# Optimization experiments

Hardware: AMD Instinct MI355X
Metric: run time of the kernel (lower is better)

Reference implementation:

```python
import jax, jax.numpy as jnp
import numpy as np

B, L, D, H, T = 1024, 50, 4, 512, 30


def _lstm_cell(x, h, c, W_ih, W_hh, b_ih, b_hh):
    # PyTorch LSTM gate order: i, f, g, o
    g = x @ W_ih.T + b_ih + h @ W_hh.T + b_hh
    i, f, gg, o = jnp.split(g, 4, axis=-1)
    c = jax.nn.sigmoid(f) * c + jax.nn.sigmoid(i) * jnp.tanh(gg)
    h = jax.nn.sigmoid(o) * jnp.tanh(c)
    return h, c


def setup_inputs() -> dict:
    key = jax.random.key(0)
    ks = jax.random.split(key, 16)
    s = 0.05
    return {
        "input_tensor": jax.random.normal(ks[0], (B, L, D), jnp.float32),
        "target_len": T,
        "enc_W_ih": jax.random.normal(ks[1], (4 * H, D), jnp.float32) * s,
        "enc_W_hh": jax.random.normal(ks[2], (4 * H, H), jnp.float32) * s,
        "enc_b_ih": jax.random.normal(ks[3], (4 * H,), jnp.float32) * s,
        "enc_b_hh": jax.random.normal(ks[4], (4 * H,), jnp.float32) * s,
        "attn_W": jax.random.normal(ks[5], (L, H + D), jnp.float32) * s,
        "attn_b": jax.random.normal(ks[6], (L,), jnp.float32) * s,
        "comb_W": jax.random.normal(ks[7], (H, H + D), jnp.float32) * s,
        "comb_b": jax.random.normal(ks[8], (H,), jnp.float32) * s,
        "dec_W_ih": jax.random.normal(ks[9], (4 * H, H), jnp.float32) * s,
        "dec_W_hh": jax.random.normal(ks[10], (4 * H, H), jnp.float32) * s,
        "dec_b_ih": jax.random.normal(ks[11], (4 * H,), jnp.float32) * s,
        "dec_b_hh": jax.random.normal(ks[12], (4 * H,), jnp.float32) * s,
        "out_W": jax.random.normal(ks[13], (D, H), jnp.float32) * s,
        "out_b": jax.random.normal(ks[14], (D,), jnp.float32) * s,
    }


def reference(input_tensor, target_len, enc_W_ih, enc_W_hh, enc_b_ih, enc_b_hh,
              attn_W, attn_b, comb_W, comb_b,
              dec_W_ih, dec_W_hh, dec_b_ih, dec_b_hh, out_W, out_b):
    b = input_tensor.shape[0]

    # ---- encoder LSTM over input_len steps ----
    def enc_step(carry, x_t):
        h, c = carry
        h, c = _lstm_cell(x_t, h, c, enc_W_ih, enc_W_hh, enc_b_ih, enc_b_hh)
        return (h, c), h

    h0 = jnp.zeros((b, H), input_tensor.dtype)
    (h_enc, c_enc), enc_hs = jax.lax.scan(enc_step, (h0, h0),
                                          jnp.swapaxes(input_tensor, 0, 1))
    encoder_outputs = jnp.swapaxes(enc_hs, 0, 1)  # [B, L, H]

    # ---- recursive attention decoder over target_len steps ----
    def dec_step(carry, _):
        h, c, x = carry
        # faithful to torch: h.reshape(h.shape[1], -1).transpose(1, 0)
        h_r = jnp.transpose(h.reshape(H, -1))  # [B, H] (memory reinterpret)
        attn_logits = jnp.concatenate([x, h_r], axis=1) @ attn_W.T + attn_b
        attn_weights = jax.nn.softmax(attn_logits, axis=1)        # [B, L]
        attn_applied = jnp.einsum('bl,blh->bh', attn_weights, encoder_outputs)
        comb = jnp.concatenate([x, attn_applied], axis=1) @ comb_W.T + comb_b
        comb = jax.nn.relu(comb)                                  # [B, H]
        h, c = _lstm_cell(comb, h, c, dec_W_ih, dec_W_hh, dec_b_ih, dec_b_hh)
        pred = h @ out_W.T + out_b                                # [B, D]
        return (h, c, pred), pred

    dec_in0 = input_tensor[:, -1, :]
    _, preds = jax.lax.scan(dec_step, (h_enc, c_enc, dec_in0), None,
                            length=target_len)
    return jnp.swapaxes(preds, 0, 1)  # [B, target_len, D]
```

## Files before the change

kernel.cpp:

```cpp
#include <hip/hip_runtime.h>
#include <hip/hip_bf16.h>

#define Bsz   1024
#define Lseq  50
#define Din   4
#define Hd    512
#define Tlen  30

typedef __hip_bfloat16 bf16;
typedef short s16x8 __attribute__((ext_vector_type(8)));
typedef short s16x4 __attribute__((ext_vector_type(4)));
typedef float f32x4 __attribute__((ext_vector_type(4)));

__device__ __forceinline__ float bf2f(bf16 x){ return __bfloat162float(x); }
__device__ __forceinline__ bf16  f2bf(float x){ return __float2bfloat16(x); }
__device__ __forceinline__ float bfbits2f(short u){
    union { unsigned int ui; float f; } v;
    v.ui = ((unsigned int)(unsigned short)u) << 16;
    return v.f;
}
__device__ __forceinline__ short f2bfbits(float x){
    bf16 h = f2bf(x); short s; __builtin_memcpy(&s, &h, 2); return s;
}
__device__ __forceinline__ float sigm(float x){ return 1.0f/(1.0f + __expf(-x)); }

#define OFF_ABUF0   (0u)
#define OFF_ABUF1   (2u<<20)
#define OFF_CBUF    (4u<<20)
#define OFF_HF32    (6u<<20)
#define OFF_ATTNAP  (8u<<20)
#define OFF_XDEC    (9u<<20)
#define OFF_FLAG    ((9u<<20) + (16u<<10))
#define OFF_COMBWR  ((9u<<20) + (32u<<10))
#define OFF_ATTNWR  ((9u<<20) + (600u<<10))
#define OFF_WCACHE  (10u<<20)
#define OFF_ENCOUT  (18u<<20)

#define WC_INPUT 0
#define WC_EWIH  204800
#define WC_EWHH  212992
#define WC_EBIH  1261568
#define WC_EBHH  1263616
#define WC_AW    1265664
#define WC_AB    1291464
#define WC_CW    1291520
#define WC_CB    1555712
#define WC_DWIH  1556224
#define WC_DWHH  2604800
#define WC_DBIH  3653376
#define WC_DBHH  3655424
#define WC_OW    3657472
#define WC_OB    3659520
#define WC_TOTAL 3659524

__device__ __constant__ int WOFF[15] = {
    WC_INPUT, WC_EWIH, WC_EWHH, WC_EBIH, WC_EBHH, WC_AW, WC_AB, WC_CW,
    WC_CB, WC_DWIH, WC_DWHH, WC_DBIH, WC_DBHH, WC_OW, WC_OB };
__device__ __constant__ int WNUM[15] = {
    204800, 8192, 1048576, 2048, 2048, 25800, 50, 264192,
    512, 1048576, 1048576, 2048, 2048, 2048, 4 };

struct Ptrs15 { const void* p[15]; };

__global__ void probe_kernel(const unsigned int* __restrict__ w, int* flag){
    __shared__ int cnt;
    if (threadIdx.x == 0) cnt = 0;
    __syncthreads();
    int c = 0;
    for (int i = threadIdx.x; i < 4096; i += 256){
        unsigned e = (w[i] >> 7) & 0xFFu;
        c += (e >= 0x80u) ? 1 : 0;
    }
    atomicAdd(&cnt, c);
    __syncthreads();
    if (threadIdx.x == 0) *flag = (cnt > 400) ? 1 : 0;
}

__global__ __launch_bounds__(256) void convert_kernel(
    Ptrs15 srcs, const int* __restrict__ flag, bf16* __restrict__ dst)
{
    const int f = *flag;
    for (int idx = blockIdx.x*256 + threadIdx.x; idx < WC_TOTAL;
         idx += gridDim.x*256){
        int a = 0;
#pragma unroll
        for (int j = 1; j < 15; ++j) if (idx >= WOFF[j]) a = j;
        const int local = idx - WOFF[a];
        if (local >= WNUM[a]) continue;
        bf16 v;
        if (f) v = f2bf(((const float*)srcs.p[a])[local]);
        else   v = ((const bf16*)srcs.p[a])[local];
        dst[idx] = v;
    }
}

__global__ __launch_bounds__(256) void setup_kernel(
    bf16* __restrict__ Abuf0, bf16* __restrict__ Abuf1,
    float* __restrict__ cbuf, bf16* __restrict__ combWr,
    bf16* __restrict__ attnWr,
    const bf16* __restrict__ cWc, const bf16* __restrict__ aWc)
{
    const unsigned idx = blockIdx.x*256u + threadIdx.x;
    if (idx < (unsigned)Bsz*Hd){
        const unsigned row = idx >> 9, col = idx & (Hd-1);
        const bf16 z = f2bf(0.0f);
        Abuf0[(size_t)row*1024 + Hd + col] = z;
        Abuf1[(size_t)row*1024 + Hd + col] = z;
        cbuf[idx] = 0.0f;
    }
    if (idx < (unsigned)Hd*Hd)
        combWr[idx] = cWc[(size_t)(idx >> 9)*(Hd+Din) + Din + (idx & (Hd-1))];
    if (idx < (unsigned)Lseq*Hd)
        attnWr[idx] = aWc[(size_t)(idx >> 9)*(Hd+Din) + Din + (idx & (Hd-1))];
}

template<bool TWO, bool HASX, bool WENC>
__global__ __launch_bounds__(512, 2) void gates_kernel(
    const bf16* __restrict__ A, int lda,
    const bf16* __restrict__ W1, const bf16* __restrict__ W2,
    const bf16* __restrict__ bih, const bf16* __restrict__ bhh,
    const bf16* __restrict__ Wx,
    const bf16* __restrict__ xsrc, int ldx,
    float* __restrict__ cbuf,
    bf16* __restrict__ hout,
    bf16* __restrict__ hout2, int ldh2,
    float* __restrict__ hf32)
{
    const int wg = blockIdx.x;
    const int mt = wg >> 4, nt = wg & 15;
    const int bm0 = mt << 6, hc0 = nt << 5;
    const int tid = threadIdx.x;
    const int wave = tid >> 6, lane = tid & 63;
    const int wm = wave >> 1, wn = wave & 1;
    const int quad = lane >> 4, l15 = lane & 15;

    const int arow = bm0 + wm*16 + l15;
    int ng[4];
#pragma unroll
    for (int an = 0; an < 4; ++an){
        const int n = wn*64 + an*16 + l15;
        ng[an] = (n & 3)*Hd + hc0 + (n >> 2);
    }

    float bias[4];
#pragma unroll
    for (int an = 0; an < 4; ++an)
        bias[an] = bf2f(bih[ng[an]]) + bf2f(bhh[ng[an]]);
    float xv[4][4], wxv[4][4];
    if (HASX){
#pragma unroll
        for (int r = 0; r < 4; ++r){
            const int m = bm0 + wm*16 + quad*4 + r;
            const s16x4 t = *reinterpret_cast<const s16x4*>(xsrc + (size_t)m*ldx);
#pragma unroll
            for (int d = 0; d < 4; ++d) xv[r][d] = bfbits2f(t[d]);
        }
#pragma unroll
        for (int an = 0; an < 4; ++an){
            const s16x4 t = *reinterpret_cast<const s16x4*>(Wx + (size_t)ng[an]*Din);
#pragma unroll
            for (int d = 0; d < 4; ++d) wxv[an][d] = bfbits2f(t[d]);
        }
    }

    f32x4 acc[4];
#pragma unroll
    for (int an = 0; an < 4; ++an) acc[an] = (f32x4)0.0f;

    const bf16* Ab = A + (size_t)arow*lda + quad*8;
    const bf16* wbase[2] = { W1, W2 };
#pragma unroll
    for (int h = 0; h < (TWO ? 2 : 1); ++h){
        const bf16* Wb = wbase[h];
        const bf16* Ah = Ab + h*Hd;
#pragma unroll
        for (int kk = 0; kk < 16; ++kk){
            const int k = kk*32 + quad*8;
            s16x8 bfr[4];
#pragma unroll
            for (int an = 0; an < 4; ++an)
                bfr[an] = *reinterpret_cast<const s16x8*>(Wb + (size_t)ng[an]*Hd + k);
            const s16x8 afr = *reinterpret_cast<const s16x8*>(Ah + kk*32);
#pragma unroll
            for (int an = 0; an < 4; ++an)
                acc[an] = __builtin_amdgcn_mfma_f32_16x16x32_bf16(afr, bfr[an], acc[an], 0, 0, 0);
        }
    }

    const int lbase = lane & ~3;
#pragma unroll
    for (int an = 0; an < 4; ++an){
        const int n = wn*64 + an*16 + l15;
        const int hcol = hc0 + (n >> 2);
#pragma unroll
        for (int r = 0; r < 4; ++r){
            const int m = bm0 + wm*16 + quad*4 + r;
            float gv = acc[an][r] + bias[an];
            if (HASX)
                gv += xv[r][0]*wxv[an][0] + xv[r][1]*wxv[an][1]
                    + xv[r][2]*wxv[an][2] + xv[r][3]*wxv[an][3];
            const float gi = __shfl(gv, lbase+0);
            const float gf = __shfl(gv, lbase+1);
            const float gg = __shfl(gv, lbase+2);
            const float go = __shfl(gv, lbase+3);
            if ((lane & 3) == 0){
                const size_t ci = (size_t)m*Hd + hcol;
                const float cn = sigm(gf)*cbuf[ci] + sigm(gi)*tanhf(gg);
                cbuf[ci] = cn;
                const float hv = sigm(go)*tanhf(cn);
                const bf16 hb = f2bf(hv);
                hout[(size_t)m*1024 + hcol] = hb;
                hf32[ci] = hv;
                if (WENC) hout2[(size_t)m*ldh2 + hcol] = hb;
            }
        }
    }
}

__global__ __launch_bounds__(256) void comb_kernel(
    const bf16* __restrict__ A,
    const bf16* __restrict__ Wr,
    const bf16* __restrict__ combW,
    const bf16* __restrict__ combB,
    const bf16* __restrict__ xdec,
    bf16* __restrict__ out)
{
    const int wg = blockIdx.x;
    const int mt = wg >> 3, nt = wg & 7;
    const int bm0 = mt << 5, n0 = nt << 6;
    const int tid = threadIdx.x;
    const int wave = tid >> 6, lane = tid & 63;
    const int wm = wave >> 1, wn = wave & 1;
    const int quad = lane >> 4, l15 = lane & 15;

    const int arow = bm0 + wm*16 + l15;
    int ncol[2];
#pragma unroll
    for (int j = 0; j < 2; ++j) ncol[j] = n0 + wn*32 + j*16 + l15;

    float bias[2], wxv[2][4];
#pragma unroll
    for (int j = 0; j < 2; ++j){
        bias[j] = bf2f(combB[ncol[j]]);
        const s16x4 t = *reinterpret_cast<const s16x4*>(combW + (size_t)ncol[j]*(Hd+Din));
#pragma unroll
        for (int d = 0; d < 4; ++d) wxv[j][d] = bfbits2f(t[d]);
    }
    float xv[4][4];
#pragma unroll
    for (int r = 0; r < 4; ++r){
        const int m = bm0 + wm*16 + quad*4 + r;
        const s16x4 t = *reinterpret_cast<const s16x4*>(xdec + (size_t)m*Din);
#pragma unroll
        for (int d = 0; d < 4; ++d) xv[r][d] = bfbits2f(t[d]);
    }

    f32x4 acc[2];
#pragma unroll
    for (int j = 0; j < 2; ++j) acc[j] = (f32x4)0.0f;

    const bf16* Ab = A + (size_t)arow*Hd + quad*8;
#pragma unroll
    for (int kk = 0; kk < 16; ++kk){
        const int k = kk*32 + quad*8;
        s16x8 bfr[2];
#pragma unroll
        for (int j = 0; j < 2; ++j)
            bfr[j] = *reinterpret_cast<const s16x8*>(Wr + (size_t)ncol[j]*Hd + k);
        const s16x8 afr = *reinterpret_cast<const s16x8*>(Ab + kk*32);
#pragma unroll
        for (int j = 0; j < 2; ++j)
            acc[j] = __builtin_amdgcn_mfma_f32_16x16x32_bf16(afr, bfr[j], acc[j], 0, 0, 0);
    }

#pragma unroll
    for (int j = 0; j < 2; ++j){
        const int n = ncol[j];
#pragma unroll
        for (int r = 0; r < 4; ++r){
            const int m = bm0 + wm*16 + quad*4 + r;
            float v = acc[j][r] + bias[j]
                    + xv[r][0]*wxv[j][0] + xv[r][1]*wxv[j][1]
                    + xv[r][2]*wxv[j][2] + xv[r][3]*wxv[j][3];
            v = fmaxf(v, 0.0f);
            out[(size_t)m*1024 + n] = f2bf(v);
        }
    }
}

__global__ __launch_bounds__(256) void attn_kernel(
    int t, const int* __restrict__ flagp,
    const bf16* __restrict__ input,
    const float* __restrict__ hf32,
    const bf16* __restrict__ enc_out,
    const bf16* __restrict__ attnW,
    const bf16* __restrict__ attnWr,
    const bf16* __restrict__ attnB,
    const bf16* __restrict__ outW,  const bf16* __restrict__ outB,
    void* __restrict__ dout,
    bf16* __restrict__ xdec,
    bf16* __restrict__ attnap)
{
    __shared__ float hr_s[4][Hd];
    const int f32out = *flagp;
    const int wave = threadIdx.x >> 6, lane = threadIdx.x & 63;
    const int b = blockIdx.x*4 + wave;

    float x0, x1, x2, x3;
    if (t == 0){
        const bf16* xp = input + ((size_t)b*Lseq + (Lseq-1))*Din;
        x0 = bf2f(xp[0]); x1 = bf2f(xp[1]); x2 = bf2f(xp[2]); x3 = bf2f(xp[3]);
    } else {
        float p0=0.f, p1=0.f, p2=0.f, p3=0.f;
        const float* hb = hf32 + (size_t)b*Hd;
        for (int k=lane; k<Hd; k+=64){
            const float hv = hb[k];
            p0 += hv*bf2f(outW[0*Hd+k]);
            p1 += hv*bf2f(outW[1*Hd+k]);
            p2 += hv*bf2f(outW[2*Hd+k]);
            p3 += hv*bf2f(outW[3*Hd+k]);
        }
#pragma unroll
        for (int off=32; off; off>>=1){
            p0 += __shfl_down(p0, off); p1 += __shfl_down(p1, off);
            p2 += __shfl_down(p2, off); p3 += __shfl_down(p3, off);
        }
        x0 = __shfl(p0,0) + bf2f(outB[0]);
        x1 = __shfl(p1,0) + bf2f(outB[1]);
        x2 = __shfl(p2,0) + bf2f(outB[2]);
        x3 = __shfl(p3,0) + bf2f(outB[3]);
        if (lane == 0){
            const size_t o = ((size_t)b*Tlen + (t-1))*Din;
            if (f32out){
                float* dp = (float*)dout + o;
                dp[0]=x0; dp[1]=x1; dp[2]=x2; dp[3]=x3;
            } else {
                bf16* dp = (bf16*)dout + o;
                dp[0]=f2bf(x0); dp[1]=f2bf(x1); dp[2]=f2bf(x2); dp[3]=f2bf(x3);
            }
        }
    }
    if (lane == 0){
        bf16* xp = xdec + (size_t)b*Din;
        xp[0]=f2bf(x0); xp[1]=f2bf(x1); xp[2]=f2bf(x2); xp[3]=f2bf(x3);
    }

    const int s = b >> 9, p = b & (Hd-1);
    for (int j=lane; j<Hd; j+=64)
        hr_s[wave][j] = hf32[(size_t)(2*j + s)*Hd + p];
    __syncthreads();

    float logit = -3.0e38f;
    if (lane < Lseq){
        float a0 = bf2f(attnB[lane]);
        {
            const bf16* wx = attnW + (size_t)lane*(Hd+Din);
            a0 += x0*bf2f(wx[0]) + x1*bf2f(wx[1]) + x2*bf2f(wx[2]) + x3*bf2f(wx[3]);
        }
        float a1 = 0.f, a2 = 0.f, a3 = 0.f;
        const bf16* wr = attnWr + (size_t)lane*Hd;
        for (int j = 0; j < Hd; j += 16){
            float acc4[4] = {0.f,0.f,0.f,0.f};
#pragma unroll
            for (int q = 0; q < 4; ++q){
                const float4 hv = *reinterpret_cast<const float4*>(&hr_s[wave][j + q*4]);
                const s16x4 wv = *reinterpret_cast<const s16x4*>(wr + j + q*4);
                acc4[q] = hv.x*bfbits2f(wv[0]) + hv.y*bfbits2f(wv[1])
                        + hv.z*bfbits2f(wv[2]) + hv.w*bfbits2f(wv[3]);
            }
            a0 += acc4[0]; a1 += acc4[1]; a2 += acc4[2]; a3 += acc4[3];
        }
        logit = (a0 + a1) + (a2 + a3);
    }
    float mx = logit;
#pragma unroll
    for (int off=32; off; off>>=1) mx = fmaxf(mx, __shfl_xor(mx, off));
    const float e = (lane < Lseq) ? __expf(logit - mx) : 0.0f;
    float se = e;
#pragma unroll
    for (int off=32; off; off>>=1) se += __shfl_xor(se, off);
    const float myaw = e / se;

    float acc8[8] = {0.f,0.f,0.f,0.f,0.f,0.f,0.f,0.f};
    const bf16* eb = enc_out + (size_t)b*Lseq*Hd + lane*8;
    for (int l=0; l<Lseq; ++l){
        const float w = __shfl(myaw, l);
        const s16x8 ch = *reinterpret_cast<const s16x8*>(eb + (size_t)l*Hd);
#pragma unroll
        for (int q=0; q<8; ++q) acc8[q] += w * bfbits2f(ch[q]);
    }
    s16x8 ov;
#pragma unroll
    for (int q=0; q<8; ++q) ov[q] = f2bfbits(acc8[q]);
    *reinterpret_cast<s16x8*>(attnap + (size_t)b*Hd + lane*8) = ov;
}

__global__ __launch_bounds__(256) void pred_kernel(
    const int* __restrict__ flagp,
    const float* __restrict__ hf32,
    const bf16* __restrict__ outW, const bf16* __restrict__ outB,
    void* __restrict__ dout)
{
    const int f32out = *flagp;
    const int wave = threadIdx.x >> 6, lane = threadIdx.x & 63;
    const int b = blockIdx.x*4 + wave;
    float p0=0.f, p1=0.f, p2=0.f, p3=0.f;
    const float* hb = hf32 + (size_t)b*Hd;
    for (int k=lane; k<Hd; k+=64){
        const float hv = hb[k];
        p0 += hv*bf2f(outW[0*Hd+k]);
        p1 += hv*bf2f(outW[1*Hd+k]);
        p2 += hv*bf2f(outW[2*Hd+k]);
        p3 += hv*bf2f(outW[3*Hd+k]);
    }
#pragma unroll
    for (int off=32; off; off>>=1){
        p0 += __shfl_down(p0, off); p1 += __shfl_down(p1, off);
        p2 += __shfl_down(p2, off); p3 += __shfl_down(p3, off);
    }
    if (lane == 0){
        const size_t o = ((size_t)b*Tlen + (Tlen-1))*Din;
        const float r0 = p0 + bf2f(outB[0]), r1 = p1 + bf2f(outB[1]);
        const float r2 = p2 + bf2f(outB[2]), r3 = p3 + bf2f(outB[3]);
        if (f32out){
            float* dp = (float*)dout + o;
            dp[0]=r0; dp[1]=r1; dp[2]=r2; dp[3]=r3;
        } else {
            bf16* dp = (bf16*)dout + o;
            dp[0]=f2bf(r0); dp[1]=f2bf(r1); dp[2]=f2bf(r2); dp[3]=f2bf(r3);
        }
    }
}

extern "C" void kernel_launch(void* const* d_in, const int* in_sizes, int n_in,
                              void* d_out, int out_size, void* d_ws, size_t ws_size,
                              hipStream_t stream)
{
    char* ws = (char*)d_ws;
    bf16*  Abuf0   = (bf16*)(ws + OFF_ABUF0);
    bf16*  Abuf1   = (bf16*)(ws + OFF_ABUF1);
    float* cbuf    = (float*)(ws + OFF_CBUF);
    float* hf32    = (float*)(ws + OFF_HF32);
    bf16*  attnap  = (bf16*)(ws + OFF_ATTNAP);
    bf16*  xdec    = (bf16*)(ws + OFF_XDEC);
    int*   flag    = (int*)(ws + OFF_FLAG);
    bf16*  combWr  = (bf16*)(ws + OFF_COMBWR);
    bf16*  attnWr  = (bf16*)(ws + OFF_ATTNWR);
    bf16*  wc      = (bf16*)(ws + OFF_WCACHE);
    bf16*  enc_out = (bf16*)(ws + OFF_ENCOUT);

    const bf16 *c_input = wc+WC_INPUT, *c_eWih = wc+WC_EWIH, *c_eWhh = wc+WC_EWHH,
               *c_ebih = wc+WC_EBIH, *c_ebhh = wc+WC_EBHH, *c_aW = wc+WC_AW,
               *c_ab = wc+WC_AB, *c_cW = wc+WC_CW, *c_cb = wc+WC_CB,
               *c_dWih = wc+WC_DWIH, *c_dWhh = wc+WC_DWHH, *c_dbih = wc+WC_DBIH,
               *c_dbhh = wc+WC_DBHH, *c_oW = wc+WC_OW, *c_ob = wc+WC_OB;

    bf16* Abuf[2] = {Abuf0, Abuf1};

    probe_kernel<<<1, 256, 0, stream>>>((const unsigned int*)d_in[3], flag);

    Ptrs15 srcs;
    srcs.p[0]=d_in[0];  srcs.p[1]=d_in[2];  srcs.p[2]=d_in[3];  srcs.p[3]=d_in[4];
    srcs.p[4]=d_in[5];  srcs.p[5]=d_in[6];  srcs.p[6]=d_in[7];  srcs.p[7]=d_in[8];
    srcs.p[8]=d_in[9];  srcs.p[9]=d_in[10]; srcs.p[10]=d_in[11];srcs.p[11]=d_in[12];
    srcs.p[12]=d_in[13];srcs.p[13]=d_in[14];srcs.p[14]=d_in[15];
    convert_kernel<<<1024, 256, 0, stream>>>(srcs, flag, wc);

    setup_kernel<<<2048, 256, 0, stream>>>(Abuf0, Abuf1, cbuf, combWr, attnWr,
                                           c_cW, c_aW);

    for (int t = 0; t < Lseq; ++t){
        gates_kernel<false, true, true><<<256, 512, 0, stream>>>(
            Abuf[t&1] + Hd, 1024,
            c_eWhh, c_eWhh, c_ebih, c_ebhh,
            c_eWih, c_input + (size_t)t*Din, Lseq*Din,
            cbuf,
            Abuf[(t+1)&1] + Hd,
            enc_out + (size_t)t*Hd, Lseq*Hd,
            hf32);
    }

    for (int t = 0; t < Tlen; ++t){
        const int p = t & 1;
        attn_kernel<<<256, 256, 0, stream>>>(
            t, flag, c_input, hf32, enc_out, c_aW, attnWr, c_ab, c_oW, c_ob,
            d_out, xdec, attnap);
        comb_kernel<<<256, 256, 0, stream>>>(
            attnap, combWr, c_cW, c_cb, xdec, Abuf[p]);
        gates_kernel<true, false, false><<<256, 512, 0, stream>>>(
            Abuf[p], 1024,
            c_dWih, c_dWhh, c_dbih, c_dbhh,
            nullptr, nullptr, 0,
            cbuf,
            Abuf[(t+1)&1] + Hd,
            nullptr, 0,
            hf32);
    }

    pred_kernel<<<256, 256, 0, stream>>>(flag, hf32, c_oW, c_ob, d_out);
}
```

Measured before the change: 3.631 ms.

## Fuse encoder and decoder steps into one persistent kernel with grid barriers

Replaces about 140 separate launches (encoder gates, attention, comb, decoder gates, pred) with a single persistent 256-workgroup kernel that synchronises with an atomic-counter grid barrier between phases. Each workgroup keeps its slice of the recurrent weight matrix in registers across steps, so that slice is not reloaded from memory every step. The attention transposed-hidden gather is also vectorised through shared memory. This removes launch overhead and repeated weight traffic. In exchange, correctness depends on all 256 workgroups being co-resident, and the large register footprint may limit occupancy.

```diff
diff --git a/kernel.cpp b/kernel.cpp
--- a/kernel.cpp
+++ b/kernel.cpp
@@ -6,6 +6,7 @@
 #define Din   4
 #define Hd    512
 #define Tlen  30
+#define NWG   256
 
 typedef __hip_bfloat16 bf16;
 typedef short s16x8 __attribute__((ext_vector_type(8)));
@@ -31,6 +32,7 @@
 #define OFF_ATTNAP  (8u<<20)
 #define OFF_XDEC    (9u<<20)
 #define OFF_FLAG    ((9u<<20) + (16u<<10))
+#define OFF_CNT     ((9u<<20) + (20u<<10))
 #define OFF_COMBWR  ((9u<<20) + (32u<<10))
 #define OFF_ATTNWR  ((9u<<20) + (600u<<10))
 #define OFF_WCACHE  (10u<<20)
@@ -114,320 +116,410 @@
         attnWr[idx] = aWc[(size_t)(idx >> 9)*(Hd+Din) + Din + (idx & (Hd-1))];
 }
 
-template<bool TWO, bool HASX, bool WENC>
-__global__ __launch_bounds__(512, 2) void gates_kernel(
-    const bf16* __restrict__ A, int lda,
-    const bf16* __restrict__ W1, const bf16* __restrict__ W2,
-    const bf16* __restrict__ bih, const bf16* __restrict__ bhh,
-    const bf16* __restrict__ Wx,
-    const bf16* __restrict__ xsrc, int ldx,
-    float* __restrict__ cbuf,
-    bf16* __restrict__ hout,
-    bf16* __restrict__ hout2, int ldh2,
-    float* __restrict__ hf32)
+__device__ __forceinline__ void gridbar(int* cnt, int target){
+    __syncthreads();
+    if (threadIdx.x == 0){
+        __threadfence();
+        __hip_atomic_fetch_add(cnt, 1, __ATOMIC_RELEASE, __HIP_MEMORY_SCOPE_AGENT);
+        while (__hip_atomic_load(cnt, __ATOMIC_RELAXED, __HIP_MEMORY_SCOPE_AGENT) < target)
+            __builtin_amdgcn_s_sleep(2);
+        (void)__hip_atomic_load(cnt, __ATOMIC_ACQUIRE, __HIP_MEMORY_SCOPE_AGENT);
+    }
+    __syncthreads();
+}
+
+struct MegaP {
+    const bf16 *input, *eWih, *eWhh, *ebih, *ebhh;
+    const bf16 *aW, *ab, *cW, *cb, *dWih, *dWhh, *dbih, *dbhh, *oW, *ob;
+    const bf16 *combWr, *attnWr;
+    bf16 *A0, *A1, *encout, *attnap, *xdec;
+    float *cbuf, *hf32;
+    int *cnt;
+    const int *flag;
+    void *dout;
+};
+
+__global__ __launch_bounds__(512, 2) void mega_kernel(MegaP P)
 {
-    const int wg = blockIdx.x;
+    __shared__ float hr_s[4][Hd];
+    __shared__ float ctx_s[2][4][Hd];
+    __shared__ float aw_s[4][64];
+
+    const int wg = blockIdx.x, tid = threadIdx.x;
+    const int wave = tid >> 6, lane = tid & 63;
+    const int quad = lane >> 4, l15 = lane & 15;
+    const int lbase = lane & ~3;
+    const int f32out = *P.flag;
+    int bar = 0;
+
+    bf16* bufs[2] = { P.A0, P.A1 };
+
     const int mt = wg >> 4, nt = wg & 15;
     const int bm0 = mt << 6, hc0 = nt << 5;
-    const int tid = threadIdx.x;
-    const int wave = tid >> 6, lane = tid & 63;
-    const int wm = wave >> 1, wn = wave & 1;
-    const int quad = lane >> 4, l15 = lane & 15;
-
-    const int arow = bm0 + wm*16 + l15;
-    int ng[4];
-#pragma unroll
-    for (int an = 0; an < 4; ++an){
-        const int n = wn*64 + an*16 + l15;
-        ng[an] = (n & 3)*Hd + hc0 + (n >> 2);
-    }
-
-    float bias[4];
-#pragma unroll
-    for (int an = 0; an < 4; ++an)
-        bias[an] = bf2f(bih[ng[an]]) + bf2f(bhh[ng[an]]);
-    float xv[4][4], wxv[4][4];
-    if (HASX){
-#pragma unroll
-        for (int r = 0; r < 4; ++r){
-            const int m = bm0 + wm*16 + quad*4 + r;
-            const s16x4 t = *reinterpret_cast<const s16x4*>(xsrc + (size_t)m*ldx);
-#pragma unroll
-            for (int d = 0; d < 4; ++d) xv[r][d] = bfbits2f(t[d]);
-        }
-#pragma unroll
-        for (int an = 0; an < 4; ++an){
-            const s16x4 t = *reinterpret_cast<const s16x4*>(Wx + (size_t)ng[an]*Din);
-#pragma unroll
-            for (int d = 0; d < 4; ++d) wxv[an][d] = bfbits2f(t[d]);
-        }
-    }
-
-    f32x4 acc[4];
-#pragma unroll
-    for (int an = 0; an < 4; ++an) acc[an] = (f32x4)0.0f;
-
-    const bf16* Ab = A + (size_t)arow*lda + quad*8;
-    const bf16* wbase[2] = { W1, W2 };
-#pragma unroll
-    for (int h = 0; h < (TWO ? 2 : 1); ++h){
-        const bf16* Wb = wbase[h];
-        const bf16* Ah = Ab + h*Hd;
-#pragma unroll
-        for (int kk = 0; kk < 16; ++kk){
-            const int k = kk*32 + quad*8;
-            s16x8 bfr[4];
-#pragma unroll
-            for (int an = 0; an < 4; ++an)
-                bfr[an] = *reinterpret_cast<const s16x8*>(Wb + (size_t)ng[an]*Hd + k);
-            const s16x8 afr = *reinterpret_cast<const s16x8*>(Ah + kk*32);
-#pragma unroll
-            for (int an = 0; an < 4; ++an)
-                acc[an] = __builtin_amdgcn_mfma_f32_16x16x32_bf16(afr, bfr[an], acc[an], 0, 0, 0);
-        }
-    }
-
-    const int lbase = lane & ~3;
-#pragma unroll
-    for (int an = 0; an < 4; ++an){
-        const int n = wn*64 + an*16 + l15;
-        const int hcol = hc0 + (n >> 2);
-#pragma unroll
-        for (int r = 0; r < 4; ++r){
-            const int m = bm0 + wm*16 + quad*4 + r;
-            float gv = acc[an][r] + bias[an];
-            if (HASX)
-                gv += xv[r][0]*wxv[an][0] + xv[r][1]*wxv[an][1]
-                    + xv[r][2]*wxv[an][2] + xv[r][3]*wxv[an][3];
-            const float gi = __shfl(gv, lbase+0);
-            const float gf = __shfl(gv, lbase+1);
-            const float gg = __shfl(gv, lbase+2);
-            const float go = __shfl(gv, lbase+3);
-            if ((lane & 3) == 0){
-                const size_t ci = (size_t)m*Hd + hcol;
-                const float cn = sigm(gf)*cbuf[ci] + sigm(gi)*tanhf(gg);
-                cbuf[ci] = cn;
-                const float hv = sigm(go)*tanhf(cn);
-                const bf16 hb = f2bf(hv);
-                hout[(size_t)m*1024 + hcol] = hb;
-                hf32[ci] = hv;
-                if (WENC) hout2[(size_t)m*ldh2 + hcol] = hb;
-            }
-        }
-    }
-}
-
-__global__ __launch_bounds__(256) void comb_kernel(
-    const bf16* __restrict__ A,
-    const bf16* __restrict__ Wr,
-    const bf16* __restrict__ combW,
-    const bf16* __restrict__ combB,
-    const bf16* __restrict__ xdec,
-    bf16* __restrict__ out)
-{
-    const int wg = blockIdx.x;
-    const int mt = wg >> 3, nt = wg & 7;
-    const int bm0 = mt << 5, n0 = nt << 6;
-    const int tid = threadIdx.x;
-    const int wave = tid >> 6, lane = tid & 63;
-    const int wm = wave >> 1, wn = wave & 1;
-    const int quad = lane >> 4, l15 = lane & 15;
-
-    const int arow = bm0 + wm*16 + l15;
-    int ncol[2];
-#pragma unroll
-    for (int j = 0; j < 2; ++j) ncol[j] = n0 + wn*32 + j*16 + l15;
-
-    float bias[2], wxv[2][4];
+    const int wm = wave >> 2, wn = wave & 3;
+    const int arow0 = bm0 + wm*32 + l15;
+
+    int ng[2];
+#pragma unroll
+    for (int nf = 0; nf < 2; ++nf){
+        const int n = wn*32 + nf*16 + l15;
+        ng[nf] = (n & 3)*Hd + hc0 + (n >> 2);
+    }
+
+    float bias_e[2], wxv_e[2][4];
+#pragma unroll
+    for (int nf = 0; nf < 2; ++nf){
+        bias_e[nf] = bf2f(P.ebih[ng[nf]]) + bf2f(P.ebhh[ng[nf]]);
+        const s16x4 t4 = *reinterpret_cast<const s16x4*>(P.eWih + (size_t)ng[nf]*Din);
+#pragma unroll
+        for (int d = 0; d < 4; ++d) wxv_e[nf][d] = bfbits2f(t4[d]);
+    }
+
+    s16x8 breg[2][16];
+#pragma unroll
+    for (int nf = 0; nf < 2; ++nf)
+#pragma unroll
+        for (int sl = 0; sl < 16; ++sl)
+            breg[nf][sl] = *reinterpret_cast<const s16x8*>(
+                P.eWhh + (size_t)ng[nf]*Hd + sl*32 + quad*8);
+
+    for (int t = 0; t < Lseq; ++t){
+        const bf16* Ain = bufs[t&1] + Hd;
+        bf16* hout = bufs[(t+1)&1] + Hd;
+
+        f32x4 acc[2][2];
+#pragma unroll
+        for (int mf=0; mf<2; ++mf)
+#pragma unroll
+            for (int nf=0; nf<2; ++nf) acc[mf][nf] = (f32x4)0.0f;
+
+        s16x8 afr[2];
+#pragma unroll
+        for (int sl = 0; sl < 16; ++sl){
+#pragma unroll
+            for (int mf = 0; mf < 2; ++mf)
+                afr[mf] = *reinterpret_cast<const s16x8*>(
+                    Ain + (size_t)(arow0 + mf*16)*1024 + sl*32 + quad*8);
+#pragma unroll
+            for (int mf = 0; mf < 2; ++mf)
+#pragma unroll
+                for (int nf = 0; nf < 2; ++nf)
+                    acc[mf][nf] = __builtin_amdgcn_mfma_f32_16x16x32_bf16(
+                        afr[mf], breg[nf][sl], acc[mf][nf], 0, 0, 0);
+        }
+
+#pragma unroll
+        for (int mf = 0; mf < 2; ++mf){
+#pragma unroll
+            for (int r = 0; r < 4; ++r){
+                const int m = bm0 + wm*32 + mf*16 + quad*4 + r;
+                const s16x4 xt = *reinterpret_cast<const s16x4*>(
+                    P.input + ((size_t)m*Lseq + t)*Din);
+                float xv[4];
+#pragma unroll
+                for (int d = 0; d < 4; ++d) xv[d] = bfbits2f(xt[d]);
+#pragma unroll
+                for (int nf = 0; nf < 2; ++nf){
+                    const int n_loc = wn*32 + nf*16 + l15;
+                    float gv = acc[mf][nf][r] + bias_e[nf]
+                             + xv[0]*wxv_e[nf][0] + xv[1]*wxv_e[nf][1]
+                             + xv[2]*wxv_e[nf][2] + xv[3]*wxv_e[nf][3];
+                    const float gi = __shfl(gv, lbase+0);
+                    const float gf = __shfl(gv, lbase+1);
+                    const float gg = __shfl(gv, lbase+2);
+                    const float go = __shfl(gv, lbase+3);
+                    if ((lane & 3) == 0){
+                        const int hcol = hc0 + (n_loc >> 2);
+                        const size_t ci = (size_t)m*Hd + hcol;
+                        const float cn = sigm(gf)*P.cbuf[ci] + sigm(gi)*tanhf(gg);
+                        P.cbuf[ci] = cn;
+                        const float hv = sigm(go)*tanhf(cn);
+                        hout[(size_t)m*1024 + hcol] = f2bf(hv);
+                        P.hf32[ci] = hv;
+                        P.encout[((size_t)m*Lseq + t)*Hd + hcol] = f2bf(hv);
+                    }
+                }
+            }
+        }
+        gridbar(P.cnt, (++bar)*NWG);
+    }
+
+#pragma unroll
+    for (int nf = 0; nf < 2; ++nf)
+#pragma unroll
+        for (int sl = 0; sl < 16; ++sl)
+            breg[nf][sl] = *reinterpret_cast<const s16x8*>(
+                P.dWih + (size_t)ng[nf]*Hd + sl*32 + quad*8);
+
+    float bias_d[2];
+#pragma unroll
+    for (int nf = 0; nf < 2; ++nf)
+        bias_d[nf] = bf2f(P.dbih[ng[nf]]) + bf2f(P.dbhh[ng[nf]]);
+
+    const int b0 = wg*4;
+    const int s_uni = b0 >> 9;
+    const int p0 = b0 & (Hd-1);
+
+    const int cmt = wg & 31, cnt2 = wg >> 5;
+    const int cbm0 = cmt << 5, cn0 = cnt2 << 6;
+    const int cwm = (wave & 3) >> 1, cwn = wave & 1;
+    const int carow = cbm0 + cwm*16 + l15;
+    int ncol[2]; float bias_c[2], wxv_c[2][4];
 #pragma unroll
     for (int j = 0; j < 2; ++j){
-        bias[j] = bf2f(combB[ncol[j]]);
-        const s16x4 t = *reinterpret_cast<const s16x4*>(combW + (size_t)ncol[j]*(Hd+Din));
-#pragma unroll
-        for (int d = 0; d < 4; ++d) wxv[j][d] = bfbits2f(t[d]);
-    }
-    float xv[4][4];
-#pragma unroll
-    for (int r = 0; r < 4; ++r){
-        const int m = bm0 + wm*16 + quad*4 + r;
-        const s16x4 t = *reinterpret_cast<const s16x4*>(xdec + (size_t)m*Din);
-#pragma unroll
-        for (int d = 0; d < 4; ++d) xv[r][d] = bfbits2f(t[d]);
-    }
-
-    f32x4 acc[2];
-#pragma unroll
-    for (int j = 0; j < 2; ++j) acc[j] = (f32x4)0.0f;
-
-    const bf16* Ab = A + (size_t)arow*Hd + quad*8;
-#pragma unroll
-    for (int kk = 0; kk < 16; ++kk){
-        const int k = kk*32 + quad*8;
-        s16x8 bfr[2];
-#pragma unroll
-        for (int j = 0; j < 2; ++j)
-            bfr[j] = *reinterpret_cast<const s16x8*>(Wr + (size_t)ncol[j]*Hd + k);
-        const s16x8 afr = *reinterpret_cast<const s16x8*>(Ab + kk*32);
-#pragma unroll
-        for (int j = 0; j < 2; ++j)
-            acc[j] = __builtin_amdgcn_mfma_f32_16x16x32_bf16(afr, bfr[j], acc[j], 0, 0, 0);
-    }
-
-#pragma unroll
-    for (int j = 0; j < 2; ++j){
-        const int n = ncol[j];
-#pragma unroll
-        for (int r = 0; r < 4; ++r){
-            const int m = bm0 + wm*16 + quad*4 + r;
-            float v = acc[j][r] + bias[j]
-                    + xv[r][0]*wxv[j][0] + xv[r][1]*wxv[j][1]
-                    + xv[r][2]*wxv[j][2] + xv[r][3]*wxv[j][3];
-            v = fmaxf(v, 0.0f);
-            out[(size_t)m*1024 + n] = f2bf(v);
-        }
-    }
-}
-
-__global__ __launch_bounds__(256) void attn_kernel(
-    int t, const int* __restrict__ flagp,
-    const bf16* __restrict__ input,
-    const float* __restrict__ hf32,
-    const bf16* __restrict__ enc_out,
-    const bf16* __restrict__ attnW,
-    const bf16* __restrict__ attnWr,
-    const bf16* __restrict__ attnB,
-    const bf16* __restrict__ outW,  const bf16* __restrict__ outB,
-    void* __restrict__ dout,
-    bf16* __restrict__ xdec,
-    bf16* __restrict__ attnap)
-{
-    __shared__ float hr_s[4][Hd];
-    const int f32out = *flagp;
-    const int wave = threadIdx.x >> 6, lane = threadIdx.x & 63;
-    const int b = blockIdx.x*4 + wave;
-
-    float x0, x1, x2, x3;
-    if (t == 0){
-        const bf16* xp = input + ((size_t)b*Lseq + (Lseq-1))*Din;
-        x0 = bf2f(xp[0]); x1 = bf2f(xp[1]); x2 = bf2f(xp[2]); x3 = bf2f(xp[3]);
-    } else {
-        float p0=0.f, p1=0.f, p2=0.f, p3=0.f;
-        const float* hb = hf32 + (size_t)b*Hd;
-        for (int k=lane; k<Hd; k+=64){
+        ncol[j] = cn0 + cwn*32 + j*16 + l15;
+        bias_c[j] = bf2f(P.cb[ncol[j]]);
+        const s16x4 t4 = *reinterpret_cast<const s16x4*>(P.cW + (size_t)ncol[j]*(Hd+Din));
+#pragma unroll
+        for (int d = 0; d < 4; ++d) wxv_c[j][d] = bfbits2f(t4[d]);
+    }
+
+    for (int t = 0; t < Tlen; ++t){
+        const int p = t & 1;
+
+        {
+            const int j = tid;
+            const float4 hv4 = *reinterpret_cast<const float4*>(
+                P.hf32 + (size_t)(2*j + s_uni)*Hd + p0);
+            hr_s[0][j] = hv4.x; hr_s[1][j] = hv4.y;
+            hr_s[2][j] = hv4.z; hr_s[3][j] = hv4.w;
+        }
+        __syncthreads();
+
+        if (wave < 4){
+            const int b = b0 + wave;
+            float x0, x1, x2, x3;
+            if (t == 0){
+                const bf16* xp = P.input + ((size_t)b*Lseq + (Lseq-1))*Din;
+                x0 = bf2f(xp[0]); x1 = bf2f(xp[1]); x2 = bf2f(xp[2]); x3 = bf2f(xp[3]);
+            } else {
+                float q0=0.f, q1=0.f, q2=0.f, q3=0.f;
+                const float* hb = P.hf32 + (size_t)b*Hd;
+                for (int k = lane; k < Hd; k += 64){
+                    const float hv = hb[k];
+                    q0 += hv*bf2f(P.oW[k]);
+                    q1 += hv*bf2f(P.oW[Hd+k]);
+                    q2 += hv*bf2f(P.oW[2*Hd+k]);
+                    q3 += hv*bf2f(P.oW[3*Hd+k]);
+                }
+#pragma unroll
+                for (int off = 32; off; off >>= 1){
+                    q0 += __shfl_down(q0, off); q1 += __shfl_down(q1, off);
+                    q2 += __shfl_down(q2, off); q3 += __shfl_down(q3, off);
+                }
+                x0 = __shfl(q0,0) + bf2f(P.ob[0]);
+                x1 = __shfl(q1,0) + bf2f(P.ob[1]);
+                x2 = __shfl(q2,0) + bf2f(P.ob[2]);
+                x3 = __shfl(q3,0) + bf2f(P.ob[3]);
+                if (lane == 0){
+                    const size_t o = ((size_t)b*Tlen + (t-1))*Din;
+                    if (f32out){
+                        float* dp = (float*)P.dout + o;
+                        dp[0]=x0; dp[1]=x1; dp[2]=x2; dp[3]=x3;
+                    } else {
+                        bf16* dp = (bf16*)P.dout + o;
+                        dp[0]=f2bf(x0); dp[1]=f2bf(x1); dp[2]=f2bf(x2); dp[3]=f2bf(x3);
+                    }
+                }
+            }
+            if (lane == 0){
+                bf16* xp = P.xdec + (size_t)b*Din;
+                xp[0]=f2bf(x0); xp[1]=f2bf(x1); xp[2]=f2bf(x2); xp[3]=f2bf(x3);
+            }
+
+            float logit = -3.0e38f;
+            if (lane < Lseq){
+                float a0 = bf2f(P.ab[lane]);
+                {
+                    const bf16* wx = P.aW + (size_t)lane*(Hd+Din);
+                    a0 += x0*bf2f(wx[0]) + x1*bf2f(wx[1]) + x2*bf2f(wx[2]) + x3*bf2f(wx[3]);
+                }
+                float a1 = 0.f, a2 = 0.f, a3 = 0.f;
+                const bf16* wr = P.attnWr + (size_t)lane*Hd;
+                for (int j = 0; j < Hd; j += 16){
+                    float t4[4] = {0.f,0.f,0.f,0.f};
+#pragma unroll
+                    for (int q = 0; q < 4; ++q){
+                        const float4 hv = *reinterpret_cast<const float4*>(&hr_s[wave][j + q*4]);
+                        const s16x4 wv = *reinterpret_cast<const s16x4*>(wr + j + q*4);
+                        t4[q] = hv.x*bfbits2f(wv[0]) + hv.y*bfbits2f(wv[1])
+                              + hv.z*bfbits2f(wv[2]) + hv.w*bfbits2f(wv[3]);
+                    }
+                    a0 += t4[0]; a1 += t4[1]; a2 += t4[2]; a3 += t4[3];
+                }
+                logit = (a0 + a1) + (a2 + a3);
+            }
+            float mx = logit;
+#pragma unroll
+            for (int off = 32; off; off >>= 1) mx = fmaxf(mx, __shfl_xor(mx, off));
+            const float e = (lane < Lseq) ? __expf(logit - mx) : 0.0f;
+            float se = e;
+#pragma unroll
+            for (int off = 32; off; off >>= 1) se += __shfl_xor(se, off);
+            if (lane < 64) aw_s[wave][lane] = e / se;
+        }
+        __syncthreads();
+
+        {
+            const int r = wave & 3, half = wave >> 2;
+            const int b = b0 + r;
+            float acc8[8] = {0.f,0.f,0.f,0.f,0.f,0.f,0.f,0.f};
+            const bf16* eb = P.encout + (size_t)b*Lseq*Hd + lane*8;
+            for (int i = 0; i < 25; ++i){
+                const int l = half*25 + i;
+                const float w = aw_s[r][l];
+                const s16x8 ch = *reinterpret_cast<const s16x8*>(eb + (size_t)l*Hd);
+#pragma unroll
+                for (int q = 0; q < 8; ++q) acc8[q] += w * bfbits2f(ch[q]);
+            }
+            float* cp = &ctx_s[half][r][lane*8];
+            *reinterpret_cast<float4*>(cp)     = make_float4(acc8[0],acc8[1],acc8[2],acc8[3]);
+            *reinterpret_cast<float4*>(cp + 4) = make_float4(acc8[4],acc8[5],acc8[6],acc8[7]);
+        }
+        __syncthreads();
+
+        if (wave < 4){
+            const int b = b0 + wave;
+            s16x8 ov;
+#pragma unroll
+            for (int q = 0; q < 8; ++q)
+                ov[q] = f2bfbits(ctx_s[0][wave][lane*8+q] + ctx_s[1][wave][lane*8+q]);
+            *reinterpret_cast<s16x8*>(P.attnap + (size_t)b*Hd + lane*8) = ov;
+        }
+        gridbar(P.cnt, (++bar)*NWG);
+
+        if (wave < 4){
+            f32x4 cacc[2];
+#pragma unroll
+            for (int j = 0; j < 2; ++j) cacc[j] = (f32x4)0.0f;
+            const bf16* Ab = P.attnap + (size_t)carow*Hd + quad*8;
+#pragma unroll
+            for (int kk = 0; kk < 16; ++kk){
+                s16x8 bfr[2];
+#pragma unroll
+                for (int j = 0; j < 2; ++j)
+                    bfr[j] = *reinterpret_cast<const s16x8*>(
+                        P.combWr + (size_t)ncol[j]*Hd + kk*32 + quad*8);
+                const s16x8 afr2 = *reinterpret_cast<const s16x8*>(Ab + kk*32);
+#pragma unroll
+                for (int j = 0; j < 2; ++j)
+                    cacc[j] = __builtin_amdgcn_mfma_f32_16x16x32_bf16(
+                        afr2, bfr[j], cacc[j], 0, 0, 0);
+            }
+            bf16* outp = bufs[p];
+#pragma unroll
+            for (int j = 0; j < 2; ++j){
+#pragma unroll
+                for (int r = 0; r < 4; ++r){
+                    const int m = cbm0 + cwm*16 + quad*4 + r;
+                    const s16x4 xt = *reinterpret_cast<const s16x4*>(P.xdec + (size_t)m*Din);
+                    float v = cacc[j][r] + bias_c[j]
+                            + bfbits2f(xt[0])*wxv_c[j][0] + bfbits2f(xt[1])*wxv_c[j][1]
+                            + bfbits2f(xt[2])*wxv_c[j][2] + bfbits2f(xt[3])*wxv_c[j][3];
+                    v = fmaxf(v, 0.0f);
+                    outp[(size_t)m*1024 + ncol[j]] = f2bf(v);
+                }
+            }
+        }
+        gridbar(P.cnt, (++bar)*NWG);
+
+        {
+            const bf16* Ain = bufs[p];
+            bf16* hout = bufs[p^1] + Hd;
+            f32x4 acc[2][2];
+#pragma unroll
+            for (int mf=0; mf<2; ++mf)
+#pragma unroll
+                for (int nf=0; nf<2; ++nf) acc[mf][nf] = (f32x4)0.0f;
+
+            s16x8 afr[2], bfr[2];
+#pragma unroll
+            for (int sl = 0; sl < 16; ++sl){
+#pragma unroll
+                for (int mf = 0; mf < 2; ++mf)
+                    afr[mf] = *reinterpret_cast<const s16x8*>(
+                        Ain + (size_t)(arow0 + mf*16)*1024 + sl*32 + quad*8);
+#pragma unroll
+                for (int mf = 0; mf < 2; ++mf)
+#pragma unroll
+                    for (int nf = 0; nf < 2; ++nf)
+                        acc[mf][nf] = __builtin_amdgcn_mfma_f32_16x16x32_bf16(
+                            afr[mf], breg[nf][sl], acc[mf][nf], 0, 0, 0);
+            }
+#pragma unroll
+            for (int sl = 0; sl < 16; ++sl){
+#pragma unroll
+                for (int nf = 0; nf < 2; ++nf)
+                    bfr[nf] = *reinterpret_cast<const s16x8*>(
+                        P.dWhh + (size_t)ng[nf]*Hd + sl*32 + quad*8);
+#pragma unroll
+                for (int mf = 0; mf < 2; ++mf)
+                    afr[mf] = *reinterpret_cast<const s16x8*>(
+                        Ain + (size_t)(arow0 + mf*16)*1024 + Hd + sl*32 + quad*8);
+#pragma unroll
+                for (int mf = 0; mf < 2; ++mf)
+#pragma unroll
+                    for (int nf = 0; nf < 2; ++nf)
+                        acc[mf][nf] = __builtin_amdgcn_mfma_f32_16x16x32_bf16(
+                            afr[mf], bfr[nf], acc[mf][nf], 0, 0, 0);
+            }
+
+#pragma unroll
+            for (int mf = 0; mf < 2; ++mf){
+#pragma unroll
+                for (int r = 0; r < 4; ++r){
+                    const int m = bm0 + wm*32 + mf*16 + quad*4 + r;
+#pragma unroll
+                    for (int nf = 0; nf < 2; ++nf){
+                        const int n_loc = wn*32 + nf*16 + l15;
+                        float gv = acc[mf][nf][r] + bias_d[nf];
+                        const float gi = __shfl(gv, lbase+0);
+                        const float gf = __shfl(gv, lbase+1);
+                        const float gg = __shfl(gv, lbase+2);
+                        const float go = __shfl(gv, lbase+3);
+                        if ((lane & 3) == 0){
+                            const int hcol = hc0 + (n_loc >> 2);
+                            const size_t ci = (size_t)m*Hd + hcol;
+                            const float cn = sigm(gf)*P.cbuf[ci] + sigm(gi)*tanhf(gg);
+                            P.cbuf[ci] = cn;
+                            const float hv = sigm(go)*tanhf(cn);
+                            hout[(size_t)m*1024 + hcol] = f2bf(hv);
+                            P.hf32[ci] = hv;
+                        }
+                    }
+                }
+            }
+        }
+        gridbar(P.cnt, (++bar)*NWG);
+    }
+
+    if (wave < 4){
+        const int b = b0 + wave;
+        float q0=0.f, q1=0.f, q2=0.f, q3=0.f;
+        const float* hb = P.hf32 + (size_t)b*Hd;
+        for (int k = lane; k < Hd; k += 64){
             const float hv = hb[k];
-            p0 += hv*bf2f(outW[0*Hd+k]);
-            p1 += hv*bf2f(outW[1*Hd+k]);
-            p2 += hv*bf2f(outW[2*Hd+k]);
-            p3 += hv*bf2f(outW[3*Hd+k]);
-        }
-#pragma unroll
-        for (int off=32; off; off>>=1){
-            p0 += __shfl_down(p0, off); p1 += __shfl_down(p1, off);
-            p2 += __shfl_down(p2, off); p3 += __shfl_down(p3, off);
-        }
-        x0 = __shfl(p0,0) + bf2f(outB[0]);
-        x1 = __shfl(p1,0) + bf2f(outB[1]);
-        x2 = __shfl(p2,0) + bf2f(outB[2]);
-        x3 = __shfl(p3,0) + bf2f(outB[3]);
+            q0 += hv*bf2f(P.oW[k]);
+            q1 += hv*bf2f(P.oW[Hd+k]);
+            q2 += hv*bf2f(P.oW[2*Hd+k]);
+            q3 += hv*bf2f(P.oW[3*Hd+k]);
+        }
+#pragma unroll
+        for (int off = 32; off; off >>= 1){
+            q0 += __shfl_down(q0, off); q1 += __shfl_down(q1, off);
+            q2 += __shfl_down(q2, off); q3 += __shfl_down(q3, off);
+        }
         if (lane == 0){
-            const size_t o = ((size_t)b*Tlen + (t-1))*Din;
+            const size_t o = ((size_t)b*Tlen + (Tlen-1))*Din;
+            const float r0 = q0 + bf2f(P.ob[0]), r1 = q1 + bf2f(P.ob[1]);
+            const float r2 = q2 + bf2f(P.ob[2]), r3 = q3 + bf2f(P.ob[3]);
             if (f32out){
-                float* dp = (float*)dout + o;
-                dp[0]=x0; dp[1]=x1; dp[2]=x2; dp[3]=x3;
+                float* dp = (float*)P.dout + o;
+                dp[0]=r0; dp[1]=r1; dp[2]=r2; dp[3]=r3;
             } else {
-                bf16* dp = (bf16*)dout + o;
-                dp[0]=f2bf(x0); dp[1]=f2bf(x1); dp[2]=f2bf(x2); dp[3]=f2bf(x3);
-            }
-        }
-    }
-    if (lane == 0){
-        bf16* xp = xdec + (size_t)b*Din;
-        xp[0]=f2bf(x0); xp[1]=f2bf(x1); xp[2]=f2bf(x2); xp[3]=f2bf(x3);
-    }
-
-    const int s = b >> 9, p = b & (Hd-1);
-    for (int j=lane; j<Hd; j+=64)
-        hr_s[wave][j] = hf32[(size_t)(2*j + s)*Hd + p];
-    __syncthreads();
-
-    float logit = -3.0e38f;
-    if (lane < Lseq){
-        float a0 = bf2f(attnB[lane]);
-        {
-            const bf16* wx = attnW + (size_t)lane*(Hd+Din);
-            a0 += x0*bf2f(wx[0]) + x1*bf2f(wx[1]) + x2*bf2f(wx[2]) + x3*bf2f(wx[3]);
-        }
-        float a1 = 0.f, a2 = 0.f, a3 = 0.f;
-        const bf16* wr = attnWr + (size_t)lane*Hd;
-        for (int j = 0; j < Hd; j += 16){
-            float acc4[4] = {0.f,0.f,0.f,0.f};
-#pragma unroll
-            for (int q = 0; q < 4; ++q){
-                const float4 hv = *reinterpret_cast<const float4*>(&hr_s[wave][j + q*4]);
-                const s16x4 wv = *reinterpret_cast<const s16x4*>(wr + j + q*4);
-                acc4[q] = hv.x*bfbits2f(wv[0]) + hv.y*bfbits2f(wv[1])
-                        + hv.z*bfbits2f(wv[2]) + hv.w*bfbits2f(wv[3]);
-            }
-            a0 += acc4[0]; a1 += acc4[1]; a2 += acc4[2]; a3 += acc4[3];
-        }
-        logit = (a0 + a1) + (a2 + a3);
-    }
-    float mx = logit;
-#pragma unroll
-    for (int off=32; off; off>>=1) mx = fmaxf(mx, __shfl_xor(mx, off));
-    const float e = (lane < Lseq) ? __expf(logit - mx) : 0.0f;
-    float se = e;
-#pragma unroll
-    for (int off=32; off; off>>=1) se += __shfl_xor(se, off);
-    const float myaw = e / se;
-
-    float acc8[8] = {0.f,0.f,0.f,0.f,0.f,0.f,0.f,0.f};
-    const bf16* eb = enc_out + (size_t)b*Lseq*Hd + lane*8;
-    for (int l=0; l<Lseq; ++l){
-        const float w = __shfl(myaw, l);
-        const s16x8 ch = *reinterpret_cast<const s16x8*>(eb + (size_t)l*Hd);
-#pragma unroll
-        for (int q=0; q<8; ++q) acc8[q] += w * bfbits2f(ch[q]);
-    }
-    s16x8 ov;
-#pragma unroll
-    for (int q=0; q<8; ++q) ov[q] = f2bfbits(acc8[q]);
-    *reinterpret_cast<s16x8*>(attnap + (size_t)b*Hd + lane*8) = ov;
-}
-
-__global__ __launch_bounds__(256) void pred_kernel(
-    const int* __restrict__ flagp,
-    const float* __restrict__ hf32,
-    const bf16* __restrict__ outW, const bf16* __restrict__ outB,
-    void* __restrict__ dout)
-{
-    const int f32out = *flagp;
-    const int wave = threadIdx.x >> 6, lane = threadIdx.x & 63;
-    const int b = blockIdx.x*4 + wave;
-    float p0=0.f, p1=0.f, p2=0.f, p3=0.f;
-    const float* hb = hf32 + (size_t)b*Hd;
-    for (int k=lane; k<Hd; k+=64){
-        const float hv = hb[k];
-        p0 += hv*bf2f(outW[0*Hd+k]);
-        p1 += hv*bf2f(outW[1*Hd+k]);
-        p2 += hv*bf2f(outW[2*Hd+k]);
-        p3 += hv*bf2f(outW[3*Hd+k]);
-    }
-#pragma unroll
-    for (int off=32; off; off>>=1){
-        p0 += __shfl_down(p0, off); p1 += __shfl_down(p1, off);
-        p2 += __shfl_down(p2, off); p3 += __shfl_down(p3, off);
-    }
-    if (lane == 0){
-        const size_t o = ((size_t)b*Tlen + (Tlen-1))*Din;
-        const float r0 = p0 + bf2f(outB[0]), r1 = p1 + bf2f(outB[1]);
-        const float r2 = p2 + bf2f(outB[2]), r3 = p3 + bf2f(outB[3]);
-        if (f32out){
-            float* dp = (float*)dout + o;
-            dp[0]=r0; dp[1]=r1; dp[2]=r2; dp[3]=r3;
-        } else {
-            bf16* dp = (bf16*)dout + o;
-            dp[0]=f2bf(r0); dp[1]=f2bf(r1); dp[2]=f2bf(r2); dp[3]=f2bf(r3);
+                bf16* dp = (bf16*)P.dout + o;
+                dp[0]=f2bf(r0); dp[1]=f2bf(r1); dp[2]=f2bf(r2); dp[3]=f2bf(r3);
+            }
         }
     }
 }
@@ -444,18 +536,13 @@
     bf16*  attnap  = (bf16*)(ws + OFF_ATTNAP);
     bf16*  xdec    = (bf16*)(ws + OFF_XDEC);
     int*   flag    = (int*)(ws + OFF_FLAG);
+    int*   cnt     = (int*)(ws + OFF_CNT);
     bf16*  combWr  = (bf16*)(ws + OFF_COMBWR);
     bf16*  attnWr  = (bf16*)(ws + OFF_ATTNWR);
     bf16*  wc      = (bf16*)(ws + OFF_WCACHE);
     bf16*  enc_out = (bf16*)(ws + OFF_ENCOUT);
 
-    const bf16 *c_input = wc+WC_INPUT, *c_eWih = wc+WC_EWIH, *c_eWhh = wc+WC_EWHH,
-               *c_ebih = wc+WC_EBIH, *c_ebhh = wc+WC_EBHH, *c_aW = wc+WC_AW,
-               *c_ab = wc+WC_AB, *c_cW = wc+WC_CW, *c_cb = wc+WC_CB,
-               *c_dWih = wc+WC_DWIH, *c_dWhh = wc+WC_DWHH, *c_dbih = wc+WC_DBIH,
-               *c_dbhh = wc+WC_DBHH, *c_oW = wc+WC_OW, *c_ob = wc+WC_OB;
-
-    bf16* Abuf[2] = {Abuf0, Abuf1};
+    hipMemsetAsync(cnt, 0, 64, stream);
 
     probe_kernel<<<1, 256, 0, stream>>>((const unsigned int*)d_in[3], flag);
 
@@ -467,35 +554,17 @@
     convert_kernel<<<1024, 256, 0, stream>>>(srcs, flag, wc);
 
     setup_kernel<<<2048, 256, 0, stream>>>(Abuf0, Abuf1, cbuf, combWr, attnWr,
-                                           c_cW, c_aW);
-
-    for (int t = 0; t < Lseq; ++t){
-        gates_kernel<false, true, true><<<256, 512, 0, stream>>>(
-            Abuf[t&1] + Hd, 1024,
-            c_eWhh, c_eWhh, c_ebih, c_ebhh,
-            c_eWih, c_input + (size_t)t*Din, Lseq*Din,
-            cbuf,
-            Abuf[(t+1)&1] + Hd,
-            enc_out + (size_t)t*Hd, Lseq*Hd,
-            hf32);
-    }
-
-    for (int t = 0; t < Tlen; ++t){
-        const int p = t & 1;
-        attn_kernel<<<256, 256, 0, stream>>>(
-            t, flag, c_input, hf32, enc_out, c_aW, attnWr, c_ab, c_oW, c_ob,
-            d_out, xdec, attnap);
-        comb_kernel<<<256, 256, 0, stream>>>(
-            attnap, combWr, c_cW, c_cb, xdec, Abuf[p]);
-        gates_kernel<true, false, false><<<256, 512, 0, stream>>>(
-            Abuf[p], 1024,
-            c_dWih, c_dWhh, c_dbih, c_dbhh,
-            nullptr, nullptr, 0,
-            cbuf,
-            Abuf[(t+1)&1] + Hd,
-            nullptr, 0,
-            hf32);
-    }
-
-    pred_kernel<<<256, 256, 0, stream>>>(flag, hf32, c_oW, c_ob, d_out);
-}
+                                           wc+WC_CW, wc+WC_AW);
+
+    MegaP P;
+    P.input = wc+WC_INPUT; P.eWih = wc+WC_EWIH; P.eWhh = wc+WC_EWHH;
+    P.ebih = wc+WC_EBIH;   P.ebhh = wc+WC_EBHH;
+    P.aW = wc+WC_AW;  P.ab = wc+WC_AB;  P.cW = wc+WC_CW;  P.cb = wc+WC_CB;
+    P.dWih = wc+WC_DWIH; P.dWhh = wc+WC_DWHH; P.dbih = wc+WC_DBIH; P.dbhh = wc+WC_DBHH;
+    P.oW = wc+WC_OW;  P.ob = wc+WC_OB;
+    P.combWr = combWr; P.attnWr = attnWr;
+    P.A0 = Abuf0; P.A1 = Abuf1; P.encout = enc_out; P.attnap = attnap; P.xdec = xdec;
+    P.cbuf = cbuf; P.hf32 = hf32; P.cnt = cnt; P.flag = flag; P.dout = d_out;
+
+    mega_kernel<<<NWG, 512, 0, stream>>>(P);
+}
```

Result: slower. 6.378 ms (+75.7%).
